# Optimization experiments

Measured on AMD Instinct MI355X. Metric: run time of the kernel, lower is better.

## Reference

```python
import jax, jax.numpy as jnp
import numpy as np

NUM_HEADS = 8


def setup_inputs() -> dict:
    key = jax.random.key(0)
    ks = jax.random.split(key, 6)
    B, C, H, W = 64, 512, 16, 16
    x = jax.random.normal(ks[0], (B, C, H, W), dtype=jnp.float32)
    qkv_w = jax.random.normal(ks[1], (3 * C, C), dtype=jnp.float32) * (C ** -0.5)
    qkv_b = jax.random.normal(ks[2], (3 * C,), dtype=jnp.float32) * 0.02
    out_w = jax.random.normal(ks[3], (C, C), dtype=jnp.float32) * (C ** -0.5)
    out_b = jax.random.normal(ks[4], (C,), dtype=jnp.float32) * 0.02
    rel_pos_enc = jax.random.normal(ks[5], (NUM_HEADS, 2 * 16 - 1, 2 * 16 - 1), dtype=jnp.float32) * 0.02
    return {"x": x, "qkv_w": qkv_w, "qkv_b": qkv_b, "out_w": out_w,
            "out_b": out_b, "rel_pos_enc": rel_pos_enc}


def _attention(x, qkv_w, qkv_b, out_w, out_b, rel_pos_enc):
    B, C, H, W = x.shape
    heads = rel_pos_enc.shape[0]
    hd = C // heads
    N = H * W

    # 1x1 conv qkv projection == pointwise GEMM over channels
    qkv = jnp.einsum('bchw,oc->bohw', x, qkv_w) + qkv_b[None, :, None, None]
    q, k, v = jnp.split(qkv, 3, axis=1)  # each (B, C, H, W)
    q = q.reshape(B, heads, hd, N)
    k = k.reshape(B, heads, hd, N)
    v = v.reshape(B, heads, hd, N)

    attn = jnp.einsum('bhdn,bhdm->bhnm', q, k) * (hd ** -0.5)  # (B,h,N,N)

    # gathered 2D relative position bias: bias[head,(h1,w1),(h2,w2)] =
    #   rel_pos_enc[head, h1-h2+15, w1-w2+15]
    h_idx = (jnp.arange(H)[:, None] - jnp.arange(H)[None, :]) + 16 - 1  # (H,H)
    w_idx = (jnp.arange(W)[:, None] - jnp.arange(W)[None, :]) + 16 - 1  # (W,W)
    bias = rel_pos_enc[:, h_idx[:, None, :, None], w_idx[None, :, None, :]]  # (h,H,W,H,W)
    bias = bias.reshape(heads, N, N)

    attn = jax.nn.softmax(attn + bias[None], axis=-1)
    out = jnp.einsum('bhnm,bhdm->bhdn', attn, v).reshape(B, C, H, W)
    out = jnp.einsum('bchw,oc->bohw', out, out_w) + out_b[None, :, None, None]
    return out


def reference(x, qkv_w, qkv_b, out_w, out_b, rel_pos_enc):
    return _attention(x, qkv_w, qkv_b, out_w, out_b, rel_pos_enc)
```

## Files before the change

kernel.cpp:

```cpp
#include <hip/hip_runtime.h>

typedef __attribute__((ext_vector_type(8))) short short8;
typedef __attribute__((ext_vector_type(4))) float floatx4;
typedef __attribute__((ext_vector_type(4))) int   intx4;

#define MFMA16(a,b,c) __builtin_amdgcn_mfma_f32_16x16x32_bf16((a),(b),(c),0,0,0)

static __device__ __forceinline__ unsigned short f2bf(float f){
    unsigned int u = __float_as_uint(f);
    u = (u + 0x7FFFu + ((u >> 16) & 1u)) >> 16;
    return (unsigned short)u;
}

static __device__ __forceinline__ unsigned int pkbf(float lo, float hi){
    unsigned int r;
    asm("v_cvt_pk_bf16_f32 %0, %1, %2" : "=v"(r) : "v"(lo), "v"(hi));
    return r;
}

static __device__ __forceinline__ void async16(const unsigned short* g, const unsigned short* l){
    __builtin_amdgcn_global_load_lds(
        (const __attribute__((address_space(1))) unsigned int*)g,
        (__attribute__((address_space(3))) unsigned int*)l, 16, 0, 0);
}

__global__ __launch_bounds__(256) void k_prep(const float* __restrict__ x,
                                              unsigned short* __restrict__ xT,
                                              const float* __restrict__ qkvw,
                                              unsigned short* __restrict__ wqkv,
                                              const float* __restrict__ outw,
                                              unsigned short* __restrict__ wout,
                                              const float* __restrict__ rel,
                                              unsigned short* __restrict__ Bp){
    __shared__ unsigned short tile[64][78];
    const int bid = blockIdx.x;
    const int tid = threadIdx.x;
    if (bid < 2048){
        const int c0 = (bid & 7) * 64;
        const int n0 = ((bid >> 3) & 3) * 64;
        const int b  = bid >> 5;
        const int chunk = tid & 7;
        const int r     = tid >> 3;
        const float*    src = x  + (size_t)b * 131072;
        unsigned short* dst = xT + (size_t)b * 131072;
#pragma unroll
        for (int it = 0; it < 2; ++it){
            int c = r + it * 32;
            const float* p = src + (size_t)(c0 + c) * 256 + n0 + chunk * 8;
            float4 f0 = *(const float4*)(p);
            float4 f1 = *(const float4*)(p + 4);
            short8 v;
            v[0]=(short)f2bf(f0.x); v[1]=(short)f2bf(f0.y); v[2]=(short)f2bf(f0.z); v[3]=(short)f2bf(f0.w);
            v[4]=(short)f2bf(f1.x); v[5]=(short)f2bf(f1.y); v[6]=(short)f2bf(f1.z); v[7]=(short)f2bf(f1.w);
            *(short8*)&tile[c][chunk * 8] = v;
        }
        __syncthreads();
#pragma unroll
        for (int it = 0; it < 2; ++it){
            int n = r + it * 32;
            short8 o;
#pragma unroll
            for (int e = 0; e < 8; ++e) o[e] = (short)tile[chunk * 8 + e][n];
            *(short8*)(dst + (size_t)(n0 + n) * 512 + c0 + chunk * 8) = o;
        }
    } else if (bid < 3072){
        int i = (bid - 2048) * 256 + tid;
        const float* s; unsigned short* d; int j;
        if (i < 196608){ s = qkvw; d = wqkv; j = i; }
        else { j = i - 196608; if (j >= 65536) return; s = outw; d = wout; }
        float4 f = *(const float4*)(s + (size_t)j * 4);
        uint2 v;
        v.x = (unsigned int)f2bf(f.x) | ((unsigned int)f2bf(f.y) << 16);
        v.y = (unsigned int)f2bf(f.z) | ((unsigned int)f2bf(f.w) << 16);
        *(uint2*)(d + (size_t)j * 4) = v;
    } else {
        int idx   = (bid - 3072) * 256 + tid;
        int h     = idx >> 14;
        int token = (idx >> 6) & 255;
        int key0  = (idx & 63) << 2;
        int th = token >> 4, tw = token & 15;
        int kh = key0 >> 4,  kw0 = key0 & 15;
        int base = h * 961 + (th - kh + 15) * 31 + (tw - kw0 + 15);
        float v0 = rel[base]     * 1.44269504f;
        float v1 = rel[base - 1] * 1.44269504f;
        float v2 = rel[base - 2] * 1.44269504f;
        float v3 = rel[base - 3] * 1.44269504f;
        uint2 o; o.x = pkbf(v0, v1); o.y = pkbf(v2, v3);
        *(uint2*)(Bp + (size_t)idx * 4) = o;
    }
}

__global__ __launch_bounds__(512, 2) void k_fused(const unsigned short* __restrict__ xT,
                                                  const unsigned short* __restrict__ wbf,
                                                  const float* __restrict__ qkvb,
                                                  const unsigned short* __restrict__ Bp,
                                                  unsigned short* __restrict__ ao){
    __shared__ unsigned short SH[77824];
    const int XS = 0;
    const int WS = 16384;
    const int QS = 28672;
    const int KS = 45056;
    const int VS = 61440;

    const int bid  = blockIdx.x;
    const int xcd  = bid & 7;
    const int slot = bid >> 3;
    const int b = xcd * 8 + (slot & 7);
    const int h = slot >> 3;
    const int tid  = threadIdx.x;
    const int wave = tid >> 6;
    const int lane = tid & 63;
    const int lrow = lane & 15;
    const int lgrp = lane >> 4;
    const int mq = wave >> 1;
    const int nh = wave & 1;

    floatx4 acc[4][6];
#pragma unroll
    for (int i = 0; i < 4; ++i)
#pragma unroll
        for (int j = 0; j < 6; ++j){ floatx4 z = {0.f,0.f,0.f,0.f}; acc[i][j] = z; }

    const unsigned short* xb = xT + (size_t)(b * 256) * 512;
    const unsigned short* xsrc[4]; int xdo[4];
#pragma unroll
    for (int c = 0; c < 4; ++c){
        int s   = (c * 8 + wave) * 64 + lane;
        int row = s >> 3, pch = s & 7;
        int sch = pch ^ (row & 7);
        xsrc[c] = xb + (size_t)row * 512 + sch * 8;
        xdo[c]  = (c * 8 + wave) * 512;
    }
    const unsigned short* wsrc[3]; int wdo[3];
#pragma unroll
    for (int c = 0; c < 3; ++c){
        int s   = (c * 8 + wave) * 64 + lane;
        int row = s >> 3, pch = s & 7;
        int sch = pch ^ (row & 7);
        int grow = (row >> 6) * 512 + h * 64 + (row & 63);
        wsrc[c] = wbf + (size_t)grow * 512 + sch * 8;
        wdo[c]  = (c * 8 + wave) * 512;
    }

    auto stageA = [&](int XBs, int WBs, int kk){
#pragma unroll
        for (int c = 0; c < 4; ++c) async16(xsrc[c] + kk, &SH[XBs + xdo[c]]);
#pragma unroll
        for (int c = 0; c < 3; ++c) async16(wsrc[c] + kk, &SH[WBs + wdo[c]]);
    };
    auto compA = [&](int XBs, int WBs){
#pragma unroll
        for (int ks = 0; ks < 2; ++ks){
            short8 af[4], bq[6];
#pragma unroll
            for (int mt = 0; mt < 4; ++mt){
                int row = mq * 64 + mt * 16 + lrow;
                int pch = (ks * 4 + lgrp) ^ (row & 7);
                af[mt] = *(const short8*)&SH[XBs + row * 64 + pch * 8];
            }
#pragma unroll
            for (int nt = 0; nt < 6; ++nt){
                int row = nh * 96 + nt * 16 + lrow;
                int pch = (ks * 4 + lgrp) ^ (row & 7);
                bq[nt] = *(const short8*)&SH[WBs + row * 64 + pch * 8];
            }
#pragma unroll
            for (int mt = 0; mt < 4; ++mt)
#pragma unroll
                for (int nt = 0; nt < 6; ++nt)
                    acc[mt][nt] = MFMA16(af[mt], bq[nt], acc[mt][nt]);
        }
    };

    stageA(XS, WS, 0);
    stageA(QS, KS, 64);
#pragma unroll
    for (int t2 = 0; t2 < 4; ++t2){
        asm volatile("s_waitcnt vmcnt(7)" ::: "memory");
        __builtin_amdgcn_s_barrier();
        asm volatile("" ::: "memory");
        compA(XS, WS);
        asm volatile("" ::: "memory");
        if (t2 < 3){
            __builtin_amdgcn_s_barrier();
            stageA(XS, WS, t2 * 128 + 128);
            asm volatile("s_waitcnt vmcnt(7)" ::: "memory");
        } else {
            asm volatile("s_waitcnt vmcnt(0)" ::: "memory");
        }
        __builtin_amdgcn_s_barrier();
        asm volatile("" ::: "memory");
        compA(QS, KS);
        asm volatile("" ::: "memory");
        __builtin_amdgcn_s_barrier();
        if (t2 < 3) stageA(QS, KS, t2 * 128 + 192);
    }

#pragma unroll
    for (int mt = 0; mt < 4; ++mt){
#pragma unroll
        for (int nt = 0; nt < 6; ++nt){
            int col = nh * 96 + nt * 16 + lrow;
            int seg = col >> 6, off = col & 63;
            float bv = qkvb[seg * 512 + h * 64 + off];
            int token0 = mq * 64 + mt * 16 + lgrp * 4;
            if (seg == 2){
                int lch = token0 >> 3;
                int pch = (lch & 24) | ((lch & 7) ^ (off & 7));
                uint2 vv;
                vv.x = pkbf(acc[mt][nt][0] + bv, acc[mt][nt][1] + bv);
                vv.y = pkbf(acc[mt][nt][2] + bv, acc[mt][nt][3] + bv);
                *(uint2*)&SH[VS + off * 256 + pch * 8 + (lgrp & 1) * 4] = vv;
            } else if (seg == 1){
#pragma unroll
                for (int r = 0; r < 4; ++r){
                    int token = token0 + r;
                    int kslot = (token & ~0x1C) | ((token & 4) << 2) | ((token & 0x18) >> 1);
                    int pch   = (off >> 3) ^ (kslot & 7);
                    SH[KS + kslot * 64 + pch * 8 + (off & 7)] = f2bf(acc[mt][nt][r] + bv);
                }
            } else {
#pragma unroll
                for (int r = 0; r < 4; ++r){
                    int token = token0 + r;
                    int pch   = (off >> 3) ^ (token & 7);
                    SH[QS + token * 64 + pch * 8 + (off & 7)] =
                        f2bf((acc[mt][nt][r] + bv) * 0.18033688f);
                }
            }
        }
    }
    __syncthreads();

    short8 aq[2][2];
#pragma unroll
    for (int pp = 0; pp < 2; ++pp)
#pragma unroll
        for (int kc = 0; kc < 2; ++kc){
            int row = wave * 32 + pp * 16 + lrow;
            int pch = (kc * 4 + lgrp) ^ (row & 7);
            aq[pp][kc] = *(const short8*)&SH[QS + row * 64 + pch * 8];
        }

    const unsigned short* bp0 = Bp + ((size_t)h * 256 + wave * 32 + lrow) * 256;

    floatx4 st0[16], st1[16];
    __builtin_amdgcn_s_setprio(1);
#pragma unroll
    for (int ct = 0; ct < 16; ++ct){
        int key0 = 32 * (ct >> 1) + 8 * lgrp + 4 * (ct & 1);
        uint2 bA = *(const uint2*)(bp0 + key0);
        uint2 bB = *(const uint2*)(bp0 + 4096 + key0);
        int row  = ct * 16 + lrow;
        int pch0 = lgrp ^ (row & 7);
        short8 k0 = *(const short8*)&SH[KS + row * 64 + pch0 * 8];
        short8 k1 = *(const short8*)&SH[KS + row * 64 + (pch0 ^ 4) * 8];
        floatx4 z0, z1;
        z0[0] = __uint_as_float(bA.x << 16);
        z0[1] = __uint_as_float(bA.x & 0xFFFF0000u);
        z0[2] = __uint_as_float(bA.y << 16);
        z0[3] = __uint_as_float(bA.y & 0xFFFF0000u);
        z1[0] = __uint_as_float(bB.x << 16);
        z1[1] = __uint_as_float(bB.x & 0xFFFF0000u);
        z1[2] = __uint_as_float(bB.y << 16);
        z1[3] = __uint_as_float(bB.y & 0xFFFF0000u);
        z0 = MFMA16(k0, aq[0][0], z0);
        z0 = MFMA16(k1, aq[0][1], z0);
        z1 = MFMA16(k0, aq[1][0], z1);
        z1 = MFMA16(k1, aq[1][1], z1);
        st0[ct] = z0; st1[ct] = z1;
    }
    __builtin_amdgcn_s_setprio(0);

    float inv0, inv1;
    {
        float p0=0.f,p1=0.f,p2=0.f,p3=0.f;
#pragma unroll
        for (int ct = 0; ct < 16; ++ct){
            float e0 = __builtin_amdgcn_exp2f(st0[ct][0]); st0[ct][0]=e0; p0+=e0;
            float e1 = __builtin_amdgcn_exp2f(st0[ct][1]); st0[ct][1]=e1; p1+=e1;
            float e2 = __builtin_amdgcn_exp2f(st0[ct][2]); st0[ct][2]=e2; p2+=e2;
            float e3 = __builtin_amdgcn_exp2f(st0[ct][3]); st0[ct][3]=e3; p3+=e3;
        }
        float s = (p0+p1)+(p2+p3);
        s += __shfl_xor(s, 16, 64);
        s += __shfl_xor(s, 32, 64);
        inv0 = 1.f / s;
    }
    {
        float p0=0.f,p1=0.f,p2=0.f,p3=0.f;
#pragma unroll
        for (int ct = 0; ct < 16; ++ct){
            float e0 = __builtin_amdgcn_exp2f(st1[ct][0]); st1[ct][0]=e0; p0+=e0;
            float e1 = __builtin_amdgcn_exp2f(st1[ct][1]); st1[ct][1]=e1; p1+=e1;
            float e2 = __builtin_amdgcn_exp2f(st1[ct][2]); st1[ct][2]=e2; p2+=e2;
            float e3 = __builtin_amdgcn_exp2f(st1[ct][3]); st1[ct][3]=e3; p3+=e3;
        }
        float s = (p0+p1)+(p2+p3);
        s += __shfl_xor(s, 16, 64);
        s += __shfl_xor(s, 32, 64);
        inv1 = 1.f / s;
    }

    intx4 pf0[8], pf1[8];
#pragma unroll
    for (int ms = 0; ms < 8; ++ms){
        intx4 t0_, t1_;
        t0_.x = (int)pkbf(st0[2*ms  ][0], st0[2*ms  ][1]);
        t0_.y = (int)pkbf(st0[2*ms  ][2], st0[2*ms  ][3]);
        t0_.z = (int)pkbf(st0[2*ms+1][0], st0[2*ms+1][1]);
        t0_.w = (int)pkbf(st0[2*ms+1][2], st0[2*ms+1][3]);
        pf0[ms] = t0_;
        t1_.x = (int)pkbf(st1[2*ms  ][0], st1[2*ms  ][1]);
        t1_.y = (int)pkbf(st1[2*ms  ][2], st1[2*ms  ][3]);
        t1_.z = (int)pkbf(st1[2*ms+1][0], st1[2*ms+1][1]);
        t1_.w = (int)pkbf(st1[2*ms+1][2], st1[2*ms+1][3]);
        pf1[ms] = t1_;
    }

    unsigned short* aob = ao + (size_t)(b * 256) * 512 + h * 64;
    const int n0 = wave * 32 + lrow;
    __builtin_amdgcn_s_setprio(1);
#pragma unroll
    for (int dt = 0; dt < 4; ++dt){
        floatx4 a0 = {0.f,0.f,0.f,0.f}, a1 = {0.f,0.f,0.f,0.f};
#pragma unroll
        for (int ms = 0; ms < 8; ++ms){
            int row = dt * 16 + lrow;
            int lch = ms * 4 + lgrp;
            int pch = (lch & 24) | ((lch & 7) ^ (row & 7));
            short8 vb = *(const short8*)&SH[VS + row * 256 + pch * 8];
            a0 = MFMA16(vb, __builtin_bit_cast(short8, pf0[ms]), a0);
            a1 = MFMA16(vb, __builtin_bit_cast(short8, pf1[ms]), a1);
        }
        uint2 o0, o1;
        o0.x = pkbf(a0[0] * inv0, a0[1] * inv0);
        o0.y = pkbf(a0[2] * inv0, a0[3] * inv0);
        *(uint2*)(aob + (size_t)n0 * 512 + dt * 16 + lgrp * 4) = o0;
        o1.x = pkbf(a1[0] * inv1, a1[1] * inv1);
        o1.y = pkbf(a1[2] * inv1, a1[3] * inv1);
        *(uint2*)(aob + (size_t)(n0 + 16) * 512 + dt * 16 + lgrp * 4) = o1;
    }
    __builtin_amdgcn_s_setprio(0);
}

__global__ __launch_bounds__(256, 2) void k_out(const unsigned short* __restrict__ ao,
                                                const unsigned short* __restrict__ wbf,
                                                const float* __restrict__ bias,
                                                float* __restrict__ out){
    __shared__ unsigned short Ash[2][2][128][32];
    __shared__ unsigned short Bsh[2][2][128][32];
    const int bid  = blockIdx.x;
    const int xcd  = bid & 7;
    const int slot = bid >> 3;
    const int t0 = (xcd * 16 + (slot & 15)) * 128;
    const int o0 = (slot >> 4) * 128;
    const int tid  = threadIdx.x;
    const int wave = tid >> 6;
    const int lane = tid & 63;
    const int lrow = lane & 15;
    const int wm   = (wave >> 1) * 64;
    const int wn   = (wave & 1) * 64;
    const int ld_row = wave * 32 + (lane >> 2);
    const int ld_col = (((lane & 3) ^ ((lane >> 3) & 3))) * 8;
    const int pcho = (((lane >> 4) ^ ((lrow >> 1) & 3))) * 8;

    floatx4 acc[4][4];
#pragma unroll
    for (int i = 0; i < 4; ++i)
#pragma unroll
        for (int j = 0; j < 4; ++j){ floatx4 z = {0.f,0.f,0.f,0.f}; acc[i][j] = z; }

    const unsigned short* gA = wbf + (size_t)(o0 + ld_row) * 512 + ld_col;
    const unsigned short* gB = ao  + (size_t)(t0 + ld_row) * 512 + ld_col;

    auto stage = [&](int d, int kk){
        async16(gA + kk,                 &Ash[d][0][wave * 32][0]);
        async16(gA + kk + 16 * 512,      &Ash[d][0][wave * 32 + 16][0]);
        async16(gA + kk + 32,            &Ash[d][1][wave * 32][0]);
        async16(gA + kk + 32 + 16 * 512, &Ash[d][1][wave * 32 + 16][0]);
        async16(gB + kk,                 &Bsh[d][0][wave * 32][0]);
        async16(gB + kk + 16 * 512,      &Bsh[d][0][wave * 32 + 16][0]);
        async16(gB + kk + 32,            &Bsh[d][1][wave * 32][0]);
        async16(gB + kk + 32 + 16 * 512, &Bsh[d][1][wave * 32 + 16][0]);
    };
    auto comp = [&](int d){
#pragma unroll
        for (int s = 0; s < 2; ++s){
            short8 af[4], bq[4];
#pragma unroll
            for (int mt = 0; mt < 4; ++mt) af[mt] = *(const short8*)&Ash[d][s][wm + mt*16 + lrow][pcho];
#pragma unroll
            for (int nt = 0; nt < 4; ++nt) bq[nt] = *(const short8*)&Bsh[d][s][wn + nt*16 + lrow][pcho];
#pragma unroll
            for (int mt = 0; mt < 4; ++mt)
#pragma unroll
                for (int nt = 0; nt < 4; ++nt)
                    acc[mt][nt] = MFMA16(af[mt], bq[nt], acc[mt][nt]);
        }
    };

    stage(0, 0);
    stage(1, 64);
#pragma unroll
    for (int t2 = 0; t2 < 4; ++t2){
        asm volatile("s_waitcnt vmcnt(8)" ::: "memory");
        __builtin_amdgcn_s_barrier();
        asm volatile("" ::: "memory");
        comp(0);
        asm volatile("" ::: "memory");
        if (t2 < 3){
            __builtin_amdgcn_s_barrier();
            stage(0, t2 * 128 + 128);
            asm volatile("s_waitcnt vmcnt(8)" ::: "memory");
        } else {
            asm volatile("s_waitcnt vmcnt(0)" ::: "memory");
        }
        __builtin_amdgcn_s_barrier();
        asm volatile("" ::: "memory");
        comp(1);
        asm volatile("" ::: "memory");
        __builtin_amdgcn_s_barrier();
        if (t2 < 3) stage(1, t2 * 128 + 192);
    }
#pragma unroll
    for (int mt = 0; mt < 4; ++mt){
        int orow0 = o0 + wm + mt*16 + (lane >> 4) * 4;
#pragma unroll
        for (int nt = 0; nt < 4; ++nt){
            int tcol = t0 + wn + nt*16 + lrow;
            int bb = tcol >> 8, nn = tcol & 255;
#pragma unroll
            for (int r = 0; r < 4; ++r){
                float bv = bias[orow0 + r];
                out[(size_t)(bb * 512 + orow0 + r) * 256 + nn] = acc[mt][nt][r] + bv;
            }
        }
    }
}

extern "C" void kernel_launch(void* const* d_in, const int* in_sizes, int n_in,
                              void* d_out, int out_size, void* d_ws, size_t ws_size,
                              hipStream_t stream){
    const float* x    = (const float*)d_in[0];
    const float* qkvw = (const float*)d_in[1];
    const float* qkvb = (const float*)d_in[2];
    const float* outw = (const float*)d_in[3];
    const float* outb = (const float*)d_in[4];
    const float* rel  = (const float*)d_in[5];
    float* out = (float*)d_out;

    const size_t XT_OFF = 0;
    const size_t AO_OFF = 16777216;
    const size_t W_OFF  = 33554432;
    const size_t NEED   = W_OFF + 4194304;
    if (ws_size < NEED) return;

    char* ws = (char*)d_ws;
    unsigned short* xT = (unsigned short*)(ws + XT_OFF);
    unsigned short* ao = (unsigned short*)(ws + AO_OFF);
    unsigned short* wqkv_bf = (unsigned short*)(ws + W_OFF);
    unsigned short* wout_bf = (unsigned short*)(ws + W_OFF + 2097152);
    unsigned short* Bp      = (unsigned short*)(ws + W_OFF + 2621440);

    hipLaunchKernelGGL(k_prep,  dim3(3584), dim3(256), 0, stream,
                       x, xT, qkvw, wqkv_bf, outw, wout_bf, rel, Bp);
    hipLaunchKernelGGL(k_fused, dim3(512),  dim3(512), 0, stream,
                       xT, wqkv_bf, qkvb, Bp, ao);
    hipLaunchKernelGGL(k_out,   dim3(512),  dim3(256), 0, stream,
                       ao, wout_bf, outb, out);
}
```

Measured before the change: 151.6 us.

## Pre-swizzle bias table to MFMA fragment order and prefetch it before the QKV GEMM

Result: no change. 150.6 us (-0.6%).

```diff
diff --git a/kernel.cpp b/kernel.cpp
--- a/kernel.cpp
+++ b/kernel.cpp
@@ -74,10 +74,14 @@
         v.y = (unsigned int)f2bf(f.z) | ((unsigned int)f2bf(f.w) << 16);
         *(uint2*)(d + (size_t)j * 4) = v;
     } else {
-        int idx   = (bid - 3072) * 256 + tid;
-        int h     = idx >> 14;
-        int token = (idx >> 6) & 255;
-        int key0  = (idx & 63) << 2;
+        int idx  = (bid - 3072) * 256 + tid;
+        int lane = idx & 63;
+        int ct   = (idx >> 6) & 15;
+        int pp   = (idx >> 10) & 1;
+        int wv   = (idx >> 11) & 7;
+        int h    = idx >> 14;
+        int token = wv * 32 + pp * 16 + (lane & 15);
+        int key0  = 32 * (ct >> 1) + 8 * (lane >> 4) + 4 * (ct & 1);
         int th = token >> 4, tw = token & 15;
         int kh = key0 >> 4,  kw0 = key0 & 15;
         int base = h * 961 + (th - kh + 15) * 31 + (tw - kw0 + 15);
@@ -114,6 +118,14 @@
     const int lgrp = lane >> 4;
     const int mq = wave >> 1;
     const int nh = wave & 1;
+
+    const uint2* bpw = (const uint2*)Bp + (((size_t)h * 8 + wave) * 2) * 1024 + lane;
+    uint2 bA[16], bB[16];
+#pragma unroll
+    for (int ct = 0; ct < 16; ++ct){
+        bA[ct] = bpw[ct * 64];
+        bB[ct] = bpw[(16 + ct) * 64];
+    }
 
     floatx4 acc[4][6];
 #pragma unroll
@@ -242,28 +254,23 @@
             aq[pp][kc] = *(const short8*)&SH[QS + row * 64 + pch * 8];
         }
 
-    const unsigned short* bp0 = Bp + ((size_t)h * 256 + wave * 32 + lrow) * 256;
-
     floatx4 st0[16], st1[16];
     __builtin_amdgcn_s_setprio(1);
 #pragma unroll
     for (int ct = 0; ct < 16; ++ct){
-        int key0 = 32 * (ct >> 1) + 8 * lgrp + 4 * (ct & 1);
-        uint2 bA = *(const uint2*)(bp0 + key0);
-        uint2 bB = *(const uint2*)(bp0 + 4096 + key0);
         int row  = ct * 16 + lrow;
         int pch0 = lgrp ^ (row & 7);
         short8 k0 = *(const short8*)&SH[KS + row * 64 + pch0 * 8];
         short8 k1 = *(const short8*)&SH[KS + row * 64 + (pch0 ^ 4) * 8];
         floatx4 z0, z1;
-        z0[0] = __uint_as_float(bA.x << 16);
-        z0[1] = __uint_as_float(bA.x & 0xFFFF0000u);
-        z0[2] = __uint_as_float(bA.y << 16);
-        z0[3] = __uint_as_float(bA.y & 0xFFFF0000u);
-        z1[0] = __uint_as_float(bB.x << 16);
-        z1[1] = __uint_as_float(bB.x & 0xFFFF0000u);
-        z1[2] = __uint_as_float(bB.y << 16);
-        z1[3] = __uint_as_float(bB.y & 0xFFFF0000u);
+        z0[0] = __uint_as_float(bA[ct].x << 16);
+        z0[1] = __uint_as_float(bA[ct].x & 0xFFFF0000u);
+        z0[2] = __uint_as_float(bA[ct].y << 16);
+        z0[3] = __uint_as_float(bA[ct].y & 0xFFFF0000u);
+        z1[0] = __uint_as_float(bB[ct].x << 16);
+        z1[1] = __uint_as_float(bB[ct].x & 0xFFFF0000u);
+        z1[2] = __uint_as_float(bB[ct].y << 16);
+        z1[3] = __uint_as_float(bB[ct].y & 0xFFFF0000u);
         z0 = MFMA16(k0, aq[0][0], z0);
         z0 = MFMA16(k1, aq[0][1], z0);
         z1 = MFMA16(k0, aq[1][0], z1);
```
